# Kernel optimization log

Measured on AMD Instinct MI355X. Metric: run time of the kernel, lower is better.

## Reference

```python
import jax, jax.numpy as jnp
import numpy as np

B, T, F = 32, 4096, 512
H = 512

def setup_inputs() -> dict:
    key = jax.random.key(0)
    k1, k2, k3, k4, k5 = jax.random.split(key, 5)
    enc = jax.random.normal(k1, (B, T, F), dtype=jnp.float32)
    dec = jax.random.normal(k2, (B, F), dtype=jnp.float32)
    # Dense kernels (no bias), scaled like Glorot-ish init
    W1 = jax.random.normal(k3, (F, H), dtype=jnp.float32) / np.sqrt(F)
    W2 = jax.random.normal(k4, (F, H), dtype=jnp.float32) / np.sqrt(F)
    V = jax.random.normal(k5, (H, 1), dtype=jnp.float32) / np.sqrt(H)
    return {"encoder_outputs": enc, "dec_output": dec, "W1": W1, "W2": W2, "V": V}

def reference(encoder_outputs, dec_output, W1, W2, V):
    # Bahdanau additive attention, fully vectorized over time_steps
    # (the original runs this step-by-step via K.rnn; state is unchanged,
    # so the computation is embarrassingly parallel over t).
    w1_e = jnp.einsum('btf,fh->bth', encoder_outputs, W1)   # [B,T,H]
    w2_d = jnp.einsum('bf,fh->bh', dec_output, W2)          # [B,H]
    scores = jnp.einsum('bth,h->bt', jnp.tanh(w1_e + w2_d[:, None, :]), V[:, 0])  # [B,T]
    return jax.nn.softmax(scores, axis=1)
```

## Files before the change

### kernel.cpp

```cpp
#include <hip/hip_runtime.h>
#include <hip/hip_bf16.h>

#define B_ 32
#define T_ 4096
#define F_ 512
#define H_ 512

typedef float floatx4 __attribute__((ext_vector_type(4)));
typedef short short8 __attribute__((ext_vector_type(8)));

__device__ __forceinline__ unsigned pack2_bf16(float a, float b) {
  unsigned ua = __float_as_uint(a);
  unsigned ub = __float_as_uint(b);
  ua = (ua + 0x7FFFu + ((ua >> 16) & 1u)) >> 16;
  ub = (ub + 0x7FFFu + ((ub >> 16) & 1u)) & 0xFFFF0000u;
  return ua | ub;
}

__device__ __forceinline__ unsigned short f2bf16(float a) {
  unsigned ua = __float_as_uint(a);
  return (unsigned short)((ua + 0x7FFFu + ((ua >> 16) & 1u)) >> 16);
}

__device__ __forceinline__ float tanh_fast(float x) {
  float e = __expf(2.0f * x);
  return 1.0f - __fdividef(2.0f, e + 1.0f);
}

__device__ __forceinline__ void async_load16(const void* g, void* l) {
  __builtin_amdgcn_global_load_lds(
      (const __attribute__((address_space(1))) void*)g,
      (__attribute__((address_space(3))) void*)l, 16, 0, 0);
}

__global__ __launch_bounds__(256) void prep_enc(const float* __restrict__ enc,
                                                unsigned short* __restrict__ encb) {
  const int base = blockIdx.x * 512 + threadIdx.x;
  const float4* e4 = (const float4*)enc;
  uint2* o2 = (uint2*)encb;
  const float4 a = e4[base];
  const float4 b = e4[base + 256];
  uint2 pa, pb;
  pa.x = pack2_bf16(a.x, a.y);
  pa.y = pack2_bf16(a.z, a.w);
  pb.x = pack2_bf16(b.x, b.y);
  pb.y = pack2_bf16(b.z, b.w);
  o2[base] = pa;
  o2[base + 256] = pb;
}

__global__ void prep_w1t(const float* __restrict__ W1, unsigned short* __restrict__ W1T) {
  __shared__ float tile[32][33];
  const int tx = threadIdx.x, ty = threadIdx.y;
  const int f = blockIdx.y * 32 + ty;
  const int h = blockIdx.x * 32 + tx;
  tile[ty][tx] = W1[f * H_ + h];
  __syncthreads();
  const int ho = blockIdx.x * 32 + ty;
  const int fo = blockIdx.y * 32 + tx;
  W1T[ho * F_ + fo] = f2bf16(tile[tx][ty]);
}

__global__ __launch_bounds__(128) void prep_w2d(const float* __restrict__ dec,
                                                const float* __restrict__ W2,
                                                float* __restrict__ w2d) {
  const int b = blockIdx.x;
  const int h = blockIdx.y * 128 + threadIdx.x;
  float s0 = 0.f, s1 = 0.f, s2 = 0.f, s3 = 0.f;
  for (int f = 0; f < F_; f += 4) {
    s0 += dec[b * F_ + f + 0] * W2[(f + 0) * H_ + h];
    s1 += dec[b * F_ + f + 1] * W2[(f + 1) * H_ + h];
    s2 += dec[b * F_ + f + 2] * W2[(f + 2) * H_ + h];
    s3 += dec[b * F_ + f + 3] * W2[(f + 3) * H_ + h];
  }
  w2d[b * H_ + h] = (s0 + s1) + (s2 + s3);
}

__global__ __launch_bounds__(256) void fused_score_bf16(
    const unsigned short* __restrict__ encb, const unsigned short* __restrict__ W1T,
    const float* __restrict__ w2d, const float* __restrict__ V,
    float* __restrict__ scores) {
  __shared__ __align__(16) unsigned short As[2][128 * 32];
  __shared__ __align__(16) unsigned short Bs[2][128 * 32];

  const int tid = threadIdx.x;
  const int bid = blockIdx.x;
  const int xcd = bid & 7;
  const int ii = bid >> 3;
  const int n_blk = ii & 3;
  const int m_blk = xcd + ((ii >> 2) << 3);
  const int lane = tid & 63;
  const int wave = tid >> 6;
  const int wm = wave >> 1;
  const int wn = wave & 1;
  const int quad = lane >> 4;
  const int l16 = lane & 15;

  const int srow = lane >> 2;
  const int schunk = (lane & 3) ^ ((srow + (srow >> 2)) & 3);
  const unsigned short* asrc0 =
      encb + (size_t)(m_blk * 128 + wave * 32 + srow) * F_ + schunk * 8;
  const unsigned short* asrc1 = asrc0 + 16 * F_;
  const unsigned short* bsrc0 =
      W1T + (size_t)(n_blk * 128 + wave * 32 + srow) * F_ + schunk * 8;
  const unsigned short* bsrc1 = bsrc0 + 16 * F_;
  unsigned short* adst0[2] = {&As[0][wave * 1024], &As[1][wave * 1024]};
  unsigned short* bdst0[2] = {&Bs[0][wave * 1024], &Bs[1][wave * 1024]};

  floatx4 acc[4][4];
#pragma unroll
  for (int i = 0; i < 4; i++)
#pragma unroll
    for (int j = 0; j < 4; j++) acc[i][j] = (floatx4){0.f, 0.f, 0.f, 0.f};

  const int fl = (l16 + (l16 >> 2)) & 3;
  const int slot8 = (quad ^ fl) * 8;

  async_load16(asrc0, adst0[0]);
  async_load16(asrc1, adst0[0] + 512);
  async_load16(bsrc0, bdst0[0]);
  async_load16(bsrc1, bdst0[0] + 512);
  __syncthreads();

  for (int ks = 0; ks < 16; ++ks) {
    const int cur = ks & 1;
    const int nxt = cur ^ 1;
    if (ks < 15) {
      const int k1 = (ks + 1) * 32;
      async_load16(asrc0 + k1, adst0[nxt]);
      async_load16(asrc1 + k1, adst0[nxt] + 512);
      async_load16(bsrc0 + k1, bdst0[nxt]);
      async_load16(bsrc1 + k1, bdst0[nxt] + 512);
    }
    short8 af[4], bfr[4];
#pragma unroll
    for (int i = 0; i < 4; i++)
      af[i] = *(const short8*)&As[cur][(wm * 64 + i * 16 + l16) * 32 + slot8];
#pragma unroll
    for (int j = 0; j < 4; j++)
      bfr[j] = *(const short8*)&Bs[cur][(wn * 64 + j * 16 + l16) * 32 + slot8];
#pragma unroll
    for (int i = 0; i < 4; i++)
#pragma unroll
      for (int j = 0; j < 4; j++)
        acc[i][j] = __builtin_amdgcn_mfma_f32_16x16x32_bf16(af[i], bfr[j], acc[i][j], 0, 0, 0);
    __syncthreads();
  }

  const int b = m_blk >> 5;
  float w2v[4], vv[4];
#pragma unroll
  for (int j = 0; j < 4; j++) {
    const int h = n_blk * 128 + wn * 64 + j * 16 + l16;
    w2v[j] = w2d[b * H_ + h];
    vv[j] = V[h];
  }
  float rs[4][4];
#pragma unroll
  for (int i = 0; i < 4; i++)
#pragma unroll
    for (int r = 0; r < 4; r++) {
      float s = 0.f;
#pragma unroll
      for (int j = 0; j < 4; j++) s += tanh_fast(acc[i][j][r] + w2v[j]) * vv[j];
      rs[i][r] = s;
    }
#pragma unroll
  for (int i = 0; i < 4; i++)
#pragma unroll
    for (int r = 0; r < 4; r++) {
      float s = rs[i][r];
      s += __shfl_xor(s, 1, 16);
      s += __shfl_xor(s, 2, 16);
      s += __shfl_xor(s, 4, 16);
      s += __shfl_xor(s, 8, 16);
      rs[i][r] = s;
    }
  if (l16 == 0) {
#pragma unroll
    for (int i = 0; i < 4; i++)
#pragma unroll
      for (int r = 0; r < 4; r++)
        atomicAdd(&scores[m_blk * 128 + wm * 64 + i * 16 + quad * 4 + r], rs[i][r]);
  }
}

__global__ __launch_bounds__(256, 3) void fused_score_f32(
    const float* __restrict__ enc, const unsigned short* __restrict__ W1T,
    const float* __restrict__ w2d, const float* __restrict__ V,
    float* __restrict__ scores) {
  __shared__ __align__(16) unsigned short As[2][128 * 40];
  __shared__ __align__(16) unsigned short Bs[2][128 * 32];

  const int tid = threadIdx.x;
  const int bid = blockIdx.x;
  const int xcd = bid & 7;
  const int ii = bid >> 3;
  const int n_blk = ii & 3;
  const int m_blk = xcd + ((ii >> 2) << 3);
  const int lane = tid & 63;
  const int wave = tid >> 6;
  const int wm = wave >> 1;
  const int wn = wave & 1;
  const int quad = lane >> 4;
  const int l16 = lane & 15;

  const int arow = tid >> 2;
  const int acol = (tid & 3) * 8;
  const float* aptr = enc + (size_t)(m_blk * 128 + arow) * F_ + acol;

  const int nb0 = wave * 32;
  const int bl_n = lane >> 2;
  const int bl_c = (lane & 3) ^ (bl_n & 3);
  const unsigned short* bsrc0 =
      W1T + (size_t)(n_blk * 128 + nb0 + bl_n) * F_ + bl_c * 8;
  const unsigned short* bsrc1 = bsrc0 + 16 * F_;

  floatx4 acc[4][4];
#pragma unroll
  for (int i = 0; i < 4; i++)
#pragma unroll
    for (int j = 0; j < 4; j++) acc[i][j] = (floatx4){0.f, 0.f, 0.f, 0.f};

  float4 a_pre[4];
#pragma unroll
  for (int rr = 0; rr < 2; ++rr) {
    a_pre[rr * 2 + 0] = *(const float4*)(aptr + rr * 64 * F_ + 0);
    a_pre[rr * 2 + 1] = *(const float4*)(aptr + rr * 64 * F_ + 4);
  }
#pragma unroll
  for (int rr = 0; rr < 2; ++rr) {
    uint4 pk;
    pk.x = pack2_bf16(a_pre[rr * 2].x, a_pre[rr * 2].y);
    pk.y = pack2_bf16(a_pre[rr * 2].z, a_pre[rr * 2].w);
    pk.z = pack2_bf16(a_pre[rr * 2 + 1].x, a_pre[rr * 2 + 1].y);
    pk.w = pack2_bf16(a_pre[rr * 2 + 1].z, a_pre[rr * 2 + 1].w);
    *(uint4*)&As[0][(arow + rr * 64) * 40 + acol] = pk;
  }
  async_load16(bsrc0, &Bs[0][nb0 * 32]);
  async_load16(bsrc1, &Bs[0][(nb0 + 16) * 32]);
  __syncthreads();

  for (int ks = 0; ks < 16; ++ks) {
    const int cur = ks & 1;
    const int nxt = cur ^ 1;
    if (ks < 15) {
      const int k1 = (ks + 1) * 32;
#pragma unroll
      for (int rr = 0; rr < 2; ++rr) {
        a_pre[rr * 2 + 0] = *(const float4*)(aptr + rr * 64 * F_ + k1);
        a_pre[rr * 2 + 1] = *(const float4*)(aptr + rr * 64 * F_ + k1 + 4);
      }
      async_load16(bsrc0 + k1, &Bs[nxt][nb0 * 32]);
      async_load16(bsrc1 + k1, &Bs[nxt][(nb0 + 16) * 32]);
    }
    short8 af[4], bfr[4];
#pragma unroll
    for (int i = 0; i < 4; i++)
      af[i] = *(const short8*)&As[cur][(wm * 64 + i * 16 + l16) * 40 + quad * 8];
#pragma unroll
    for (int j = 0; j < 4; j++)
      bfr[j] = *(const short8*)&Bs[cur][(wn * 64 + j * 16 + l16) * 32 +
                                        ((quad ^ (l16 & 3)) * 8)];
#pragma unroll
    for (int i = 0; i < 4; i++)
#pragma unroll
      for (int j = 0; j < 4; j++)
        acc[i][j] = __builtin_amdgcn_mfma_f32_16x16x32_bf16(af[i], bfr[j], acc[i][j], 0, 0, 0);
    if (ks < 15) {
#pragma unroll
      for (int rr = 0; rr < 2; ++rr) {
        uint4 pk;
        pk.x = pack2_bf16(a_pre[rr * 2].x, a_pre[rr * 2].y);
        pk.y = pack2_bf16(a_pre[rr * 2].z, a_pre[rr * 2].w);
        pk.z = pack2_bf16(a_pre[rr * 2 + 1].x, a_pre[rr * 2 + 1].y);
        pk.w = pack2_bf16(a_pre[rr * 2 + 1].z, a_pre[rr * 2 + 1].w);
        *(uint4*)&As[nxt][(arow + rr * 64) * 40 + acol] = pk;
      }
    }
    __syncthreads();
  }

  const int b = m_blk >> 5;
  float w2v[4], vv[4];
#pragma unroll
  for (int j = 0; j < 4; j++) {
    const int h = n_blk * 128 + wn * 64 + j * 16 + l16;
    w2v[j] = w2d[b * H_ + h];
    vv[j] = V[h];
  }
  float rs[4][4];
#pragma unroll
  for (int i = 0; i < 4; i++)
#pragma unroll
    for (int r = 0; r < 4; r++) {
      float s = 0.f;
#pragma unroll
      for (int j = 0; j < 4; j++) s += tanh_fast(acc[i][j][r] + w2v[j]) * vv[j];
      rs[i][r] = s;
    }
#pragma unroll
  for (int i = 0; i < 4; i++)
#pragma unroll
    for (int r = 0; r < 4; r++) {
      float s = rs[i][r];
      s += __shfl_xor(s, 1, 16);
      s += __shfl_xor(s, 2, 16);
      s += __shfl_xor(s, 4, 16);
      s += __shfl_xor(s, 8, 16);
      rs[i][r] = s;
    }
  if (l16 == 0) {
#pragma unroll
    for (int i = 0; i < 4; i++)
#pragma unroll
      for (int r = 0; r < 4; r++)
        atomicAdd(&scores[m_blk * 128 + wm * 64 + i * 16 + quad * 4 + r], rs[i][r]);
  }
}

__global__ __launch_bounds__(256) void softmax_rows(const float* __restrict__ scores,
                                                    float* __restrict__ out) {
  const int b = blockIdx.x;
  const int tid = threadIdx.x;
  const int wave = tid >> 6;
  __shared__ float red[4];
  float v[16];
  float mx = -1e30f;
#pragma unroll
  for (int i = 0; i < 16; i++) {
    v[i] = scores[b * T_ + i * 256 + tid];
    mx = fmaxf(mx, v[i]);
  }
#pragma unroll
  for (int o = 32; o > 0; o >>= 1) mx = fmaxf(mx, __shfl_xor(mx, o, 64));
  if ((tid & 63) == 0) red[wave] = mx;
  __syncthreads();
  mx = fmaxf(fmaxf(red[0], red[1]), fmaxf(red[2], red[3]));
  __syncthreads();
  float sum = 0.f;
#pragma unroll
  for (int i = 0; i < 16; i++) {
    v[i] = __expf(v[i] - mx);
    sum += v[i];
  }
#pragma unroll
  for (int o = 32; o > 0; o >>= 1) sum += __shfl_xor(sum, o, 64);
  if ((tid & 63) == 0) red[wave] = sum;
  __syncthreads();
  sum = (red[0] + red[1]) + (red[2] + red[3]);
  const float inv = 1.0f / sum;
#pragma unroll
  for (int i = 0; i < 16; i++) out[b * T_ + i * 256 + tid] = v[i] * inv;
}

extern "C" void kernel_launch(void* const* d_in, const int* in_sizes, int n_in,
                              void* d_out, int out_size, void* d_ws, size_t ws_size,
                              hipStream_t stream) {
  const float* enc = (const float*)d_in[0];
  const float* dec = (const float*)d_in[1];
  const float* W1 = (const float*)d_in[2];
  const float* W2 = (const float*)d_in[3];
  const float* V = (const float*)d_in[4];
  float* out = (float*)d_out;

  char* ws = (char*)d_ws;
  float* scores = (float*)ws;
  unsigned short* W1T = (unsigned short*)(ws + 524288);
  float* w2d = (float*)(ws + 1048576);
  unsigned short* encb = (unsigned short*)(ws + 2097152);

  (void)in_sizes; (void)n_in; (void)out_size;

  const size_t need = 2097152ull + (size_t)B_ * T_ * F_ * 2ull;

  hipMemsetAsync(scores, 0, B_ * T_ * sizeof(float), stream);
  prep_w1t<<<dim3(16, 16), dim3(32, 32), 0, stream>>>(W1, W1T);
  prep_w2d<<<dim3(32, 4), dim3(128), 0, stream>>>(dec, W2, w2d);
  if (ws_size >= need) {
    prep_enc<<<dim3(32768), dim3(256), 0, stream>>>(enc, encb);
    fused_score_bf16<<<dim3(4096), dim3(256), 0, stream>>>(encb, W1T, w2d, V, scores);
  } else {
    fused_score_f32<<<dim3(4096), dim3(256), 0, stream>>>(enc, W1T, w2d, V, scores);
  }
  softmax_rows<<<dim3(32), dim3(256), 0, stream>>>(scores, out);
}
```

Baseline: 511.6 us.

## Pre-swizzle operands into MFMA fragment layout and load directly from global

The encoder and W1 conversion kernels now write bf16 data in the exact per-lane MFMA fragment order. The GEMM kernel then drops its LDS double buffering and barriers and loads fragments straight from global memory with 16-byte vector loads. This removes LDS traffic and synchronisation, but reuse across waves now depends on L2/L1 caching instead of shared memory, and there is no explicit prefetch pipelining beyond an unroll of 4.

New measurement: 517.1 us. No clear change (+1.1%).

```diff
diff --git a/kernel.cpp b/kernel.cpp
--- a/kernel.cpp
+++ b/kernel.cpp
@@ -33,20 +33,25 @@
       (__attribute__((address_space(3))) void*)l, 16, 0, 0);
 }
 
-__global__ __launch_bounds__(256) void prep_enc(const float* __restrict__ enc,
-                                                unsigned short* __restrict__ encb) {
-  const int base = blockIdx.x * 512 + threadIdx.x;
-  const float4* e4 = (const float4*)enc;
-  uint2* o2 = (uint2*)encb;
-  const float4 a = e4[base];
-  const float4 b = e4[base + 256];
-  uint2 pa, pb;
-  pa.x = pack2_bf16(a.x, a.y);
-  pa.y = pack2_bf16(a.z, a.w);
-  pb.x = pack2_bf16(b.x, b.y);
-  pb.y = pack2_bf16(b.z, b.w);
-  o2[base] = pa;
-  o2[base + 256] = pb;
+
+__global__ __launch_bounds__(256) void prep_encf(const float* __restrict__ enc,
+                                                 unsigned short* __restrict__ Af) {
+  const int tid = threadIdx.x;
+  const int lane = tid & 63;
+  const int fb = blockIdx.x * 4 + (tid >> 6);
+  const int mr = fb >> 4;
+  const int c = fb & 15;
+  const int row = mr * 16 + (lane & 15);
+  const int k0 = c * 32 + (lane >> 4) * 8;
+  const float4* src = (const float4*)(enc + (size_t)row * F_ + k0);
+  const float4 x = src[0];
+  const float4 y = src[1];
+  uint4 pk;
+  pk.x = pack2_bf16(x.x, x.y);
+  pk.y = pack2_bf16(x.z, x.w);
+  pk.z = pack2_bf16(y.x, y.y);
+  pk.w = pack2_bf16(y.z, y.w);
+  *(uint4*)(Af + (size_t)fb * 512 + lane * 8) = pk;
 }
 
 __global__ void prep_w1t(const float* __restrict__ W1, unsigned short* __restrict__ W1T) {
@@ -59,6 +64,19 @@
   const int ho = blockIdx.x * 32 + ty;
   const int fo = blockIdx.y * 32 + tx;
   W1T[ho * F_ + fo] = f2bf16(tile[tx][ty]);
+}
+
+__global__ __launch_bounds__(256) void prep_w1f(const unsigned short* __restrict__ W1T,
+                                                unsigned short* __restrict__ W1f) {
+  const int tid = threadIdx.x;
+  const int lane = tid & 63;
+  const int fb = blockIdx.x * 4 + (tid >> 6);
+  const int nf = fb >> 4;
+  const int c = fb & 15;
+  const int n = nf * 16 + (lane & 15);
+  const int k0 = c * 32 + (lane >> 4) * 8;
+  const short8 v = *(const short8*)(W1T + (size_t)n * F_ + k0);
+  *(short8*)(W1f + (size_t)fb * 512 + lane * 8) = v;
 }
 
 __global__ __launch_bounds__(128) void prep_w2d(const float* __restrict__ dec,
@@ -76,13 +94,10 @@
   w2d[b * H_ + h] = (s0 + s1) + (s2 + s3);
 }
 
-__global__ __launch_bounds__(256) void fused_score_bf16(
-    const unsigned short* __restrict__ encb, const unsigned short* __restrict__ W1T,
+__global__ __launch_bounds__(256) void fused_frag(
+    const unsigned short* __restrict__ Af, const unsigned short* __restrict__ W1f,
     const float* __restrict__ w2d, const float* __restrict__ V,
     float* __restrict__ scores) {
-  __shared__ __align__(16) unsigned short As[2][128 * 32];
-  __shared__ __align__(16) unsigned short Bs[2][128 * 32];
-
   const int tid = threadIdx.x;
   const int bid = blockIdx.x;
   const int xcd = bid & 7;
@@ -96,16 +111,10 @@
   const int quad = lane >> 4;
   const int l16 = lane & 15;
 
-  const int srow = lane >> 2;
-  const int schunk = (lane & 3) ^ ((srow + (srow >> 2)) & 3);
-  const unsigned short* asrc0 =
-      encb + (size_t)(m_blk * 128 + wave * 32 + srow) * F_ + schunk * 8;
-  const unsigned short* asrc1 = asrc0 + 16 * F_;
-  const unsigned short* bsrc0 =
-      W1T + (size_t)(n_blk * 128 + wave * 32 + srow) * F_ + schunk * 8;
-  const unsigned short* bsrc1 = bsrc0 + 16 * F_;
-  unsigned short* adst0[2] = {&As[0][wave * 1024], &As[1][wave * 1024]};
-  unsigned short* bdst0[2] = {&Bs[0][wave * 1024], &Bs[1][wave * 1024]};
+  const unsigned short* abase =
+      Af + ((size_t)(m_blk * 8 + wm * 4) * 16) * 512 + lane * 8;
+  const unsigned short* bbase =
+      W1f + ((size_t)(n_blk * 8 + wn * 4) * 16) * 512 + lane * 8;
 
   floatx4 acc[4][4];
 #pragma unroll
@@ -113,38 +122,20 @@
 #pragma unroll
     for (int j = 0; j < 4; j++) acc[i][j] = (floatx4){0.f, 0.f, 0.f, 0.f};
 
-  const int fl = (l16 + (l16 >> 2)) & 3;
-  const int slot8 = (quad ^ fl) * 8;
-
-  async_load16(asrc0, adst0[0]);
-  async_load16(asrc1, adst0[0] + 512);
-  async_load16(bsrc0, bdst0[0]);
-  async_load16(bsrc1, bdst0[0] + 512);
-  __syncthreads();
-
-  for (int ks = 0; ks < 16; ++ks) {
-    const int cur = ks & 1;
-    const int nxt = cur ^ 1;
-    if (ks < 15) {
-      const int k1 = (ks + 1) * 32;
-      async_load16(asrc0 + k1, adst0[nxt]);
-      async_load16(asrc1 + k1, adst0[nxt] + 512);
-      async_load16(bsrc0 + k1, bdst0[nxt]);
-      async_load16(bsrc1 + k1, bdst0[nxt] + 512);
-    }
+#pragma unroll 4
+  for (int c = 0; c < 16; ++c) {
     short8 af[4], bfr[4];
 #pragma unroll
     for (int i = 0; i < 4; i++)
-      af[i] = *(const short8*)&As[cur][(wm * 64 + i * 16 + l16) * 32 + slot8];
+      af[i] = *(const short8*)(abase + (size_t)(i * 16 + c) * 512);
 #pragma unroll
     for (int j = 0; j < 4; j++)
-      bfr[j] = *(const short8*)&Bs[cur][(wn * 64 + j * 16 + l16) * 32 + slot8];
+      bfr[j] = *(const short8*)(bbase + (size_t)(j * 16 + c) * 512);
 #pragma unroll
     for (int i = 0; i < 4; i++)
 #pragma unroll
       for (int j = 0; j < 4; j++)
         acc[i][j] = __builtin_amdgcn_mfma_f32_16x16x32_bf16(af[i], bfr[j], acc[i][j], 0, 0, 0);
-    __syncthreads();
   }
 
   const int b = m_blk >> 5;
@@ -368,7 +359,8 @@
   float* scores = (float*)ws;
   unsigned short* W1T = (unsigned short*)(ws + 524288);
   float* w2d = (float*)(ws + 1048576);
-  unsigned short* encb = (unsigned short*)(ws + 2097152);
+  unsigned short* W1f = (unsigned short*)(ws + 1179648);
+  unsigned short* Af = (unsigned short*)(ws + 2097152);
 
   (void)in_sizes; (void)n_in; (void)out_size;
 
@@ -378,8 +370,9 @@
   prep_w1t<<<dim3(16, 16), dim3(32, 32), 0, stream>>>(W1, W1T);
   prep_w2d<<<dim3(32, 4), dim3(128), 0, stream>>>(dec, W2, w2d);
   if (ws_size >= need) {
-    prep_enc<<<dim3(32768), dim3(256), 0, stream>>>(enc, encb);
-    fused_score_bf16<<<dim3(4096), dim3(256), 0, stream>>>(encb, W1T, w2d, V, scores);
+    prep_w1f<<<dim3(128), dim3(256), 0, stream>>>(W1T, W1f);
+    prep_encf<<<dim3(32768), dim3(256), 0, stream>>>(enc, Af);
+    fused_frag<<<dim3(4096), dim3(256), 0, stream>>>(Af, W1f, w2d, V, scores);
   } else {
     fused_score_f32<<<dim3(4096), dim3(256), 0, stream>>>(enc, W1T, w2d, V, scores);
   }
```
